# Kernel optimization log

Hardware: AMD Instinct MI355X
Metric: run time of the kernel (lower is better)

The kernel has to match this reference:

```python
import jax, jax.numpy as jnp
import numpy as np

CLASS_COST = 2.0
BBOX_COST = 5.0
GIOU_COST = 2.0
ALPHA = 0.25
GAMMA = 2.0
EPS = 1e-08


def center_to_corners(b):
    # b: [..., 4] in (cx, cy, w, h) -> (x0, y0, x1, y1)
    cx, cy, w, h = b[..., 0], b[..., 1], b[..., 2], b[..., 3]
    return jnp.stack([cx - 0.5 * w, cy - 0.5 * h, cx + 0.5 * w, cy + 0.5 * h], axis=-1)


def generalized_box_iou(boxes1, boxes2):
    # boxes1: [N,4], boxes2: [M,4], corners format -> [N,M] GIoU
    area1 = (boxes1[:, 2] - boxes1[:, 0]) * (boxes1[:, 3] - boxes1[:, 1])
    area2 = (boxes2[:, 2] - boxes2[:, 0]) * (boxes2[:, 3] - boxes2[:, 1])
    lt = jnp.maximum(boxes1[:, None, :2], boxes2[None, :, :2])  # [N,M,2]
    rb = jnp.minimum(boxes1[:, None, 2:], boxes2[None, :, 2:])
    wh = jnp.clip(rb - lt, 0.0)
    inter = wh[..., 0] * wh[..., 1]  # [N,M]
    union = area1[:, None] + area2[None, :] - inter
    iou = inter / union
    lt_e = jnp.minimum(boxes1[:, None, :2], boxes2[None, :, :2])
    rb_e = jnp.maximum(boxes1[:, None, 2:], boxes2[None, :, 2:])
    wh_e = jnp.clip(rb_e - lt_e, 0.0)
    area_e = wh_e[..., 0] * wh_e[..., 1]
    return iou - (area_e - union) / area_e


def setup_inputs() -> dict:
    key = jax.random.key(0)
    k1, k2, k3, k4, k5 = jax.random.split(key, 5)
    B, Q, C, T, L = 16, 900, 512, 40, 91
    return {
        "logits": jax.random.normal(k1, (B, Q, C), dtype=jnp.float32),
        "pred_boxes": jax.random.uniform(k2, (B, Q, 4), dtype=jnp.float32),
        "label_maps": jax.random.uniform(k3, (B, L, C), dtype=jnp.float32),
        "boxes": jax.random.uniform(k4, (B, T, 4), dtype=jnp.float32),
        "class_labels": jax.random.randint(k5, (B, T), 0, L, dtype=jnp.int32),
    }


def reference(logits, pred_boxes, label_maps, boxes, class_labels):
    B, Q, C = logits.shape
    T = boxes.shape[1]
    out_prob = jax.nn.sigmoid(logits.reshape(B * Q, C))          # [BQ, C]
    out_bbox = pred_boxes.reshape(B * Q, 4)
    # gather per-batch label maps, then normalize
    lm = jax.vmap(lambda m, idx: m[idx])(label_maps, class_labels)  # [B, T, C]
    lm = lm.reshape(B * T, C)
    lm = lm / lm.sum(axis=-1, keepdims=True)
    target_bbox = boxes.reshape(B * T, 4)
    # focal-style class cost
    neg_cost = (1 - ALPHA) * out_prob ** GAMMA * (-jnp.log(1 - out_prob + EPS))
    pos_cost = ALPHA * (1 - out_prob) ** GAMMA * (-jnp.log(out_prob + EPS))
    class_cost = (pos_cost - neg_cost) @ lm.T                    # [BQ, BT]
    bbox_cost = jnp.sum(jnp.abs(out_bbox[:, None, :] - target_bbox[None, :, :]), axis=-1)
    giou_cost = -generalized_box_iou(center_to_corners(out_bbox), center_to_corners(target_bbox))
    cost = BBOX_COST * bbox_cost + CLASS_COST * class_cost + GIOU_COST * giou_cost
    return cost.reshape(B, Q, B * T)
```

## Files before the change

kernel.cpp:

```cpp
#include <hip/hip_runtime.h>
#include <hip/hip_bf16.h>

#define BQ   14400
#define BT   640
#define CD   512
#define LD   91
#define TD   40

typedef __attribute__((ext_vector_type(8))) short short8;
typedef __attribute__((ext_vector_type(4))) float f32x4;

__global__ __launch_bounds__(256) void build_lmfrag_kernel(
    const float* __restrict__ label_maps,
    const int* __restrict__ class_labels,
    __hip_bfloat16* __restrict__ Bf)
{
    __shared__ float rows[16][512];
    __shared__ float inv[16];
    int nt = blockIdx.x;
    int t  = threadIdx.x;

    #pragma unroll
    for (int e = 0; e < 8; ++e) {
        int idx4 = t + e * 256;
        int r    = idx4 >> 7;
        int c4   = idx4 & 127;
        int j    = nt * 16 + r;
        int b    = j / TD;
        int cls  = class_labels[j];
        float4 v = *(const float4*)(label_maps + ((size_t)(b * LD + cls) * CD) + c4 * 4);
        *(float4*)(&rows[r][c4 * 4]) = v;
    }
    __syncthreads();

    int w = t >> 6, l = t & 63;
    #pragma unroll
    for (int q = 0; q < 4; ++q) {
        int r = w * 4 + q;
        float s = 0.f;
        #pragma unroll
        for (int e = 0; e < 8; ++e) s += rows[r][l + e * 64];
        #pragma unroll
        for (int off = 32; off >= 1; off >>= 1) s += __shfl_down(s, off, 64);
        if (l == 0) inv[r] = __builtin_amdgcn_rcpf(s);
    }
    __syncthreads();

    int w5 = nt / 5, nf5 = nt % 5;
    #pragma unroll
    for (int e = 0; e < 4; ++e) {
        int sc = t + e * 256;
        int kb = sc >> 6;
        int ln = sc & 63;
        int o  = ln >> 4;
        int rr = ln & 15;
        float scale = inv[rr];
        union { __hip_bfloat16 h[8]; uint4 u; } pk;
        #pragma unroll
        for (int j2 = 0; j2 < 8; ++j2)
            pk.h[j2] = __float2bfloat16(rows[rr][kb * 32 + o * 8 + j2] * scale);
        size_t chunk = (size_t)(w5 * 16 + kb) * 5 + nf5;
        *(uint4*)((char*)Bf + (chunk * 64 + ln) * 16) = pk.u;
    }
}

__device__ __forceinline__ float focal_term(float x)
{
    x = fminf(fmaxf(x, -18.0f), 18.0f);
    float q   = __expf(-x);
    float s   = 1.0f + q;
    float p   = __builtin_amdgcn_rcpf(s);
    float spn = __logf(s);
    float omp = q * p;
    float pos = 0.25f * omp * omp * spn;
    float neg = 0.75f * p * p * (x + spn);
    return pos - neg;
}

__global__ __launch_bounds__(512, 2) void fused_cost_kernel(
    const float* __restrict__ logits,
    const float* __restrict__ pred_boxes,
    const __hip_bfloat16* __restrict__ Bf,
    const float* __restrict__ tboxes,
    float* __restrict__ out)
{
    __shared__ __align__(16) short A[64][512];
    __shared__ float pB[64][4];

    int t  = threadIdx.x;
    int m0 = blockIdx.x * 64;
    int l    = t & 63;
    int w    = t >> 6;
    int lrow = l & 15;
    int kg   = l >> 4;
    int r7a  = lrow & 7;

    const short8* bw = (const short8*)Bf + (size_t)w * 80 * 64 + l;

    short8 b0[5], b1[5], b2[5];
    #pragma unroll
    for (int nf = 0; nf < 5; ++nf) b0[nf] = bw[(0 * 5 + nf) * 64];
    #pragma unroll
    for (int nf = 0; nf < 5; ++nf) b1[nf] = bw[(1 * 5 + nf) * 64];

    if (t < 64) *(float4*)(&pB[t][0]) = *(const float4*)(pred_boxes + (size_t)(m0 + t) * 4);

    {
        int row = t >> 3;
        int sl  = t & 7;
        int r7  = row & 7;
        const float* lp = logits + (size_t)(m0 + row) * CD + sl * 16;
        #pragma unroll
        for (int i = 0; i < 4; ++i) {
            union { float4 v4[4]; float f[16]; } xu;
            #pragma unroll
            for (int j = 0; j < 4; ++j) xu.v4[j] = *(const float4*)(lp + i * 128 + j * 4);
            union { __hip_bfloat16 h[16]; uint4 u[2]; } pk;
            #pragma unroll
            for (int k = 0; k < 16; ++k) pk.h[k] = __float2bfloat16(focal_term(xu.f[k]));
            int o0 = sl * 2 + i * 16;
            *(uint4*)(&A[row][(o0 ^ r7) * 8])       = pk.u[0];
            *(uint4*)(&A[row][((o0 + 1) ^ r7) * 8]) = pk.u[1];
        }
    }
    __syncthreads();

    f32x4 acc[4][5] = {};
    #pragma unroll
    for (int kb = 0; kb < 16; ++kb) {
        short8* const bufs[3] = { b0, b1, b2 };
        if (kb < 14) {
            short8* nb = bufs[(kb + 2) % 3];
            #pragma unroll
            for (int nf = 0; nf < 5; ++nf) nb[nf] = bw[((kb + 2) * 5 + nf) * 64];
        }
        const short8* cb = bufs[kb % 3];
        #pragma unroll
        for (int rf = 0; rf < 4; ++rf) {
            short8 a = *(const short8*)(&A[rf * 16 + lrow][((kb * 4 + kg) ^ r7a) * 8]);
            #pragma unroll
            for (int nf = 0; nf < 5; ++nf)
                acc[rf][nf] = __builtin_amdgcn_mfma_f32_16x16x32_bf16(a, cb[nf], acc[rf][nf], 0, 0, 0);
        }
    }

    float tc[5][8];
    #pragma unroll
    for (int nf = 0; nf < 5; ++nf) {
        int cl = w * 80 + nf * 16 + lrow;
        float4 tb = *(const float4*)(tboxes + (size_t)cl * 4);
        tc[nf][0] = tb.x; tc[nf][1] = tb.y; tc[nf][2] = tb.z; tc[nf][3] = tb.w;
        tc[nf][4] = tb.x - 0.5f * tb.z;
        tc[nf][5] = tb.y - 0.5f * tb.w;
        tc[nf][6] = tb.x + 0.5f * tb.z;
        tc[nf][7] = tb.y + 0.5f * tb.w;
    }

    #pragma unroll
    for (int rf = 0; rf < 4; ++rf) {
        #pragma unroll
        for (int r = 0; r < 4; ++r) {
            int rl = rf * 16 + kg * 4 + r;
            float4 pb = *(const float4*)(&pB[rl][0]);
            float px0 = pb.x - 0.5f * pb.z, py0 = pb.y - 0.5f * pb.w;
            float px1 = pb.x + 0.5f * pb.z, py1 = pb.y + 0.5f * pb.w;
            float areaP = pb.z * pb.w;
            size_t orow = (size_t)(m0 + rl) * BT + w * 80 + lrow;
            #pragma unroll
            for (int nf = 0; nf < 5; ++nf) {
                const float* T = tc[nf];
                float bbox = fabsf(pb.x - T[0]) + fabsf(pb.y - T[1])
                           + fabsf(pb.z - T[2]) + fabsf(pb.w - T[3]);
                float iw = fminf(px1, T[6]) - fmaxf(px0, T[4]);
                float ih = fminf(py1, T[7]) - fmaxf(py0, T[5]);
                iw = fmaxf(iw, 0.0f); ih = fmaxf(ih, 0.0f);
                float inter = iw * ih;
                float uni   = areaP + T[2] * T[3] - inter;
                float ew = fmaxf(px1, T[6]) - fminf(px0, T[4]);
                float eh = fmaxf(py1, T[7]) - fminf(py0, T[5]);
                float areaE = ew * eh;
                float iou  = inter * __builtin_amdgcn_rcpf(uni);
                float gpen = (areaE - uni) * __builtin_amdgcn_rcpf(areaE);
                float giou = iou - gpen;
                float cls  = acc[rf][nf][r];
                out[orow + nf * 16] = 5.0f * bbox + 2.0f * cls - 2.0f * giou;
            }
        }
    }
}

extern "C" void kernel_launch(void* const* d_in, const int* in_sizes, int n_in,
                              void* d_out, int out_size, void* d_ws, size_t ws_size,
                              hipStream_t stream) {
    const float* logits       = (const float*)d_in[0];
    const float* pred_boxes   = (const float*)d_in[1];
    const float* label_maps   = (const float*)d_in[2];
    const float* boxes        = (const float*)d_in[3];
    const int*   class_labels = (const int*)d_in[4];
    float* out = (float*)d_out;

    __hip_bfloat16* Bf = (__hip_bfloat16*)d_ws;

    build_lmfrag_kernel<<<40, 256, 0, stream>>>(label_maps, class_labels, Bf);
    fused_cost_kernel<<<BQ / 64, 512, 0, stream>>>(logits, pred_boxes, Bf, boxes, out);
}
```

Before: 109.4 us.

## Stage label-map B fragments through double-buffered LDS via global_load_lds

Reorders the packed bf16 label-map fragments so each K-block slice is contiguous. The GEMM kernel then streams each slice into a double-buffered LDS region with async global-to-LDS loads, replacing the triple-buffered register prefetch. The goal is lower register pressure and fewer vector loads in flight inside the MFMA loop. In exchange it adds about 80KB of LDS per block, which on top of the 64KB A tile likely allows only one block per CU. It also adds a block-wide barrier on every K step, and each wave still reads only its own B columns, so there is no cross-wave reuse.

```diff
diff --git a/kernel.cpp b/kernel.cpp
--- a/kernel.cpp
+++ b/kernel.cpp
@@ -9,6 +9,12 @@
 
 typedef __attribute__((ext_vector_type(8))) short short8;
 typedef __attribute__((ext_vector_type(4))) float f32x4;
+
+__device__ __forceinline__ void gload_lds16(const void* g, void* lds) {
+    __builtin_amdgcn_global_load_lds(
+        (const __attribute__((address_space(1))) unsigned int*)g,
+        (__attribute__((address_space(3))) unsigned int*)lds, 16, 0, 0);
+}
 
 __global__ __launch_bounds__(256) void build_lmfrag_kernel(
     const float* __restrict__ label_maps,
@@ -59,7 +65,7 @@
         #pragma unroll
         for (int j2 = 0; j2 < 8; ++j2)
             pk.h[j2] = __float2bfloat16(rows[rr][kb * 32 + o * 8 + j2] * scale);
-        size_t chunk = (size_t)(w5 * 16 + kb) * 5 + nf5;
+        size_t chunk = ((size_t)kb * 8 + w5) * 5 + nf5;
         *(uint4*)((char*)Bf + (chunk * 64 + ln) * 16) = pk.u;
     }
 }
@@ -85,6 +91,7 @@
     float* __restrict__ out)
 {
     __shared__ __align__(16) short A[64][512];
+    __shared__ __align__(16) short Bb[2][20480];
     __shared__ float pB[64][4];
 
     int t  = threadIdx.x;
@@ -95,13 +102,10 @@
     int kg   = l >> 4;
     int r7a  = lrow & 7;
 
-    const short8* bw = (const short8*)Bf + (size_t)w * 80 * 64 + l;
-
-    short8 b0[5], b1[5], b2[5];
-    #pragma unroll
-    for (int nf = 0; nf < 5; ++nf) b0[nf] = bw[(0 * 5 + nf) * 64];
-    #pragma unroll
-    for (int nf = 0; nf < 5; ++nf) b1[nf] = bw[(1 * 5 + nf) * 64];
+    #pragma unroll
+    for (int i = 0; i < 5; ++i)
+        gload_lds16((const char*)Bf + (size_t)((i * 8 + w) * 64 + l) * 16,
+                    (char*)&Bb[0][0] + (i * 8 + w) * 1024);
 
     if (t < 64) *(float4*)(&pB[t][0]) = *(const float4*)(pred_boxes + (size_t)(m0 + t) * 4);
 
@@ -128,20 +132,27 @@
     f32x4 acc[4][5] = {};
     #pragma unroll
     for (int kb = 0; kb < 16; ++kb) {
-        short8* const bufs[3] = { b0, b1, b2 };
-        if (kb < 14) {
-            short8* nb = bufs[(kb + 2) % 3];
-            #pragma unroll
-            for (int nf = 0; nf < 5; ++nf) nb[nf] = bw[((kb + 2) * 5 + nf) * 64];
+        const int cur = kb & 1;
+        if (kb < 15) {
+            const char* src = (const char*)Bf + (size_t)(kb + 1) * 40960;
+            #pragma unroll
+            for (int i = 0; i < 5; ++i)
+                gload_lds16(src + (size_t)((i * 8 + w) * 64 + l) * 16,
+                            (char*)&Bb[cur ^ 1][0] + (i * 8 + w) * 1024);
         }
-        const short8* cb = bufs[kb % 3];
-        #pragma unroll
-        for (int rf = 0; rf < 4; ++rf) {
-            short8 a = *(const short8*)(&A[rf * 16 + lrow][((kb * 4 + kg) ^ r7a) * 8]);
+        short8 a[4], b[5];
+        #pragma unroll
+        for (int rf = 0; rf < 4; ++rf)
+            a[rf] = *(const short8*)(&A[rf * 16 + lrow][((kb * 4 + kg) ^ r7a) * 8]);
+        #pragma unroll
+        for (int nf = 0; nf < 5; ++nf)
+            b[nf] = *(const short8*)(&Bb[cur][((w * 5 + nf) * 64 + l) * 8]);
+        #pragma unroll
+        for (int rf = 0; rf < 4; ++rf)
             #pragma unroll
             for (int nf = 0; nf < 5; ++nf)
-                acc[rf][nf] = __builtin_amdgcn_mfma_f32_16x16x32_bf16(a, cb[nf], acc[rf][nf], 0, 0, 0);
-        }
+                acc[rf][nf] = __builtin_amdgcn_mfma_f32_16x16x32_bf16(a[rf], b[nf], acc[rf][nf], 0, 0, 0);
+        __syncthreads();
     }
 
     float tc[5][8];
```

New measurement: 111.8 us. 1.02x slower.
